# Optimization experiments

Measured on AMD Instinct MI355X. Metric: run time of the kernel, lower is better.

Reference implementation:

```python
import jax, jax.numpy as jnp
import numpy as np
from jax import lax

BOUNDARY_PER_ITERATION = [3, 2, 1, 0]  # boundary_width=4, boundary_iteration=4


def _cross_dilate(x):
    # grayscale dilation with 3x3 cross structuring element (max over center+4-neighbors)
    p = jnp.pad(x, ((0, 0), (0, 0), (1, 1), (1, 1)), constant_values=-jnp.inf)
    c = p[:, :, 1:-1, 1:-1]
    up = p[:, :, :-2, 1:-1]
    dn = p[:, :, 2:, 1:-1]
    lf = p[:, :, 1:-1, :-2]
    rt = p[:, :, 1:-1, 2:]
    return jnp.maximum(jnp.maximum(jnp.maximum(c, up), jnp.maximum(dn, lf)), rt)


def _full_erode(x):
    # grayscale erosion with full 3x3 structuring element (min over 3x3 window)
    return lax.reduce_window(x, jnp.inf, lax.min, (1, 1, 3, 3), (1, 1, 1, 1),
                             ((0, 0), (0, 0), (1, 1), (1, 1)))


def _box3_sum(x):
    # conv2d with all-ones 3x3 kernel, padding='same'
    return lax.reduce_window(x, 0.0, lax.add, (1, 1, 3, 3), (1, 1, 1, 1),
                             ((0, 0), (0, 0), (1, 1), (1, 1)))


def _find_boundaries(pred_f):
    return (_cross_dilate(pred_f) != _full_erode(pred_f)).astype(pred_f.dtype)


def _expand_boundaries(b, r):
    # dilation with diamond of radius r == r applications of cross dilation
    for _ in range(r):
        b = _cross_dilate(b)
    return b


def _gaussian_kernel_2d(n, std):
    i = np.arange(n, dtype=np.float64) - (n - 1) / 2.0
    g = np.exp(-(i ** 2) / (2.0 * std ** 2))
    g /= g.sum()
    return np.outer(g, g).astype(np.float32)  # cv2.getGaussianKernel outer product


def setup_inputs() -> dict:
    key = jax.random.key(0)
    k1, k2, k3 = jax.random.split(key, 3)
    n, c, h, w = 8, 19, 512, 512
    x = jax.random.normal(k1, (n, c, h, w), dtype=jnp.float32)
    means = jax.random.normal(k2, (c,), dtype=jnp.float32)
    std = jax.random.uniform(k3, (c,), dtype=jnp.float32) + 0.5  # positive variances
    gaussian_kernel = jnp.asarray(_gaussian_kernel_2d(7, 1.0))[None, None]  # (1,1,7,7)
    return {"x": x, "means": means, "std": std, "gaussian_kernel": gaussian_kernel}


def reference(x, means, std, gaussian_kernel):
    # max logits and prediction
    max_logits = jnp.max(x, axis=1, keepdims=True)           # (n,1,h,w)
    pred = jnp.argmax(x, axis=1, keepdims=True)              # (n,1,h,w) int
    sml = (max_logits - means[pred]) / std[pred]             # standardized max logits

    # boundary suppression
    pred_f = pred.astype(sml.dtype)
    boundaries = _find_boundaries(pred_f)
    for r in BOUNDARY_PER_ITERATION:
        expanded = _expand_boundaries(boundaries, r)
        nb_mask = (expanded == 0).astype(sml.dtype)
        sml_masked = sml * nb_mask
        sml_nb = _box3_sum(sml_masked)
        nb_cnt = _box3_sum(nb_mask)
        sml_avg = jnp.where(nb_cnt == 0, sml, sml_nb / jnp.where(nb_cnt == 0, 1.0, nb_cnt))
        sml = jnp.where(nb_mask == 0, sml_avg, sml)

    # dilated smoothing (gaussian conv, padding same)
    sml = lax.conv_general_dilated(sml, gaussian_kernel, (1, 1), 'SAME',
                                   dimension_numbers=('NCHW', 'OIHW', 'NCHW'))
    return sml, pred
```

## Files before the change

kernel.cpp:

```cpp
#include <hip/hip_runtime.h>
#include <cstdint>
#include <cstddef>

#define W_ 512
#define H_ 512
#define N_ 8
#define C_ 19
#define HW_ (W_*H_)
#define NPIX_ (N_*HW_)

#define TS  32
#define SR  46
#define SC  48
#define BR  52

typedef float   f32x4 __attribute__((ext_vector_type(4)));
typedef uint8_t u8x4  __attribute__((ext_vector_type(4)));
typedef unsigned long long u64;

__global__ __launch_bounds__(256) void k_argmax_sml(
    const float* __restrict__ x, const float* __restrict__ means,
    const float* __restrict__ stdv, float* __restrict__ sml,
    uint8_t* __restrict__ pred8, float* __restrict__ predf)
{
    __shared__ float xs[C_ * 1024];
    __shared__ float ms[C_], rs[C_];
    const int tid = threadIdx.x;
    if (tid < C_) {
        ms[tid] = means[tid];
        rs[tid] = __builtin_amdgcn_rcpf(stdv[tid]);
    }

    const int chunk = blockIdx.x;
    const int n   = chunk >> 8;
    const int p0  = (chunk & 255) << 10;
    const int wv  = tid >> 6, lane = tid & 63;
    const float* xg = x + (size_t)n * C_ * HW_ + p0;

    int cLo = wv * 5;
    int cHi = cLo + 5 > C_ ? C_ : cLo + 5;
    for (int c = cLo; c < cHi; ++c) {
        const float* g = xg + (size_t)c * HW_ + lane * 4;
        #pragma unroll
        for (int t = 0; t < 4; ++t) {
            __builtin_amdgcn_global_load_lds(
                (const __attribute__((address_space(1))) void*)(g + t * 256),
                (__attribute__((address_space(3))) void*)&xs[c * 1024 + t * 256],
                16, 0, 0);
        }
    }
    __syncthreads();

    const f32x4* xv = (const f32x4*)xs;
    f32x4 mv = xv[tid];
    int i0 = 0, i1 = 0, i2 = 0, i3 = 0;
    #pragma unroll
    for (int c = 1; c < C_; ++c) {
        f32x4 v = xv[c * 256 + tid];
        if (v[0] > mv[0]) { mv[0] = v[0]; i0 = c; }
        if (v[1] > mv[1]) { mv[1] = v[1]; i1 = c; }
        if (v[2] > mv[2]) { mv[2] = v[2]; i2 = c; }
        if (v[3] > mv[3]) { mv[3] = v[3]; i3 = c; }
    }
    const int pix = chunk * 1024 + tid * 4;
    f32x4 s, pf; u8x4 pc;
    s[0] = (mv[0] - ms[i0]) * rs[i0];  pf[0] = (float)i0;  pc[0] = (uint8_t)i0;
    s[1] = (mv[1] - ms[i1]) * rs[i1];  pf[1] = (float)i1;  pc[1] = (uint8_t)i1;
    s[2] = (mv[2] - ms[i2]) * rs[i2];  pf[2] = (float)i2;  pc[2] = (uint8_t)i2;
    s[3] = (mv[3] - ms[i3]) * rs[i3];  pf[3] = (float)i3;  pc[3] = (uint8_t)i3;
    *(f32x4*)(sml + pix) = s;
    *(u8x4*)(pred8 + pix) = pc;
    __builtin_nontemporal_store(pf, (f32x4*)(predf + pix));
}

__global__ __launch_bounds__(256) void k_bnd(
    const uint8_t* __restrict__ pred8, u64* __restrict__ bndM)
{
    int gid  = blockIdx.x * 256 + threadIdx.x;
    int lane = gid & 63;
    int wave = gid >> 6;
    int w = wave & 7;
    int y = (wave >> 3) & 511;
    int n = wave >> 12;
    int xx = w * 64 + lane;
    const uint8_t* pc = pred8 + (size_t)n * HW_ + y * W_ + xx;
    int c = pc[0];
    bool u = y > 0, d = y < H_-1, l = xx > 0, r = xx < W_-1;
    int up = u ? pc[-W_] : c;
    int dn = d ? pc[ W_] : c;
    int lf = l ? pc[-1]  : c;
    int rt = r ? pc[ 1]  : c;
    int mx = max(max(c, up), max(dn, max(lf, rt)));
    int mn = min(min(c, up), min(dn, min(lf, rt)));
    int c00 = (u && l) ? pc[-W_-1] : c;
    int c01 = (u && r) ? pc[-W_+1] : c;
    int c10 = (d && l) ? pc[ W_-1] : c;
    int c11 = (d && r) ? pc[ W_+1] : c;
    mn = min(mn, min(min(c00, c01), min(c10, c11)));
    u64 m = __ballot(mx != mn);
    if (lane == 0) bndM[((size_t)n * 512 + y) * 8 + w] = m;
}

__global__ __launch_bounds__(256) void k_fused(
    const float* __restrict__ sml_g, const u64* __restrict__ bndM,
    const float* __restrict__ gk, float* __restrict__ out)
{
    __shared__ float smlA[SR*SC];
    __shared__ float smlB[SR*SC];
    __shared__ u64 M0[BR], E1[BR], E2[BR], E3[BR], VM[BR];
    __shared__ u64 NBM[4][BR];
    __shared__ float g7[7];
    __shared__ int tACT;

    const int tid = threadIdx.x;
    const int bx = blockIdx.x, by = blockIdx.y, n = blockIdx.z;
    const int tx0 = bx * TS, ty0 = by * TS;
    const float* sg = sml_g + (size_t)n * HW_;

    if (tid == 0) tACT = 0;
    if (tid < 7) g7[tid] = gk[21 + tid] / sqrtf(gk[24]);

    if (tid < BR) {
        int gy = ty0 + tid - 10;
        int bx0 = tx0 - 10;
        u64 m = 0, vm = 0;
        if (gy >= 0 && gy < H_) {
            const u64* row = bndM + ((size_t)n * 512 + gy) * 8;
            int sft = bx0 & 63;
            int wi  = bx0 >> 6;
            u64 w0 = (wi >= 0) ? row[wi] : 0ULL;
            u64 w1 = (wi + 1 <= 7) ? row[wi + 1] : 0ULL;
            m = sft ? ((w0 >> sft) | (w1 << (64 - sft))) : w0;
            int lo = bx0 < 0 ? -bx0 : 0;
            int hi = (512 - bx0) < BR ? (512 - bx0) : BR;
            if (hi > lo) vm = ((1ULL << (hi - lo)) - 1ULL) << lo;
        }
        M0[tid] = m;
        VM[tid] = vm;
    }

    if (bx > 0 && bx < (W_/TS - 1)) {
        for (int s = tid; s < SR * (SC/4); s += 256) {
            int ly = s / (SC/4), j = s - ly * (SC/4);
            int gy = ty0 + ly - 7;
            f32x4 v = {0.f, 0.f, 0.f, 0.f};
            if ((unsigned)gy < (unsigned)H_)
                v = *(const f32x4*)(sg + (size_t)gy * W_ + (tx0 - 8) + j * 4);
            *(f32x4*)&smlA[ly * SC + j * 4] = v;
        }
    } else {
        for (int s = tid; s < SR * SC; s += 256) {
            int ly = s / SC, lx = s - ly * SC;
            int gy = ty0 + ly - 7, gx = tx0 + lx - 8;
            float v = 0.f;
            if ((unsigned)gy < (unsigned)H_ && (unsigned)gx < (unsigned)W_)
                v = sg[(size_t)gy * W_ + gx];
            smlA[ly * SC + lx] = v;
        }
    }
    __syncthreads();

    if (tid < BR) {
        u64 a = M0[tid], u = tid > 0 ? M0[tid-1] : 0, d = tid < BR-1 ? M0[tid+1] : 0;
        E1[tid] = a | (a << 1) | (a >> 1) | u | d;
    }
    __syncthreads();
    if (tid < BR) {
        u64 a = E1[tid], u = tid > 0 ? E1[tid-1] : 0, d = tid < BR-1 ? E1[tid+1] : 0;
        E2[tid] = a | (a << 1) | (a >> 1) | u | d;
    }
    __syncthreads();
    if (tid < BR) {
        u64 a = E2[tid], u = tid > 0 ? E2[tid-1] : 0, d = tid < BR-1 ? E2[tid+1] : 0;
        E3[tid] = a | (a << 1) | (a >> 1) | u | d;
    }
    __syncthreads();
    {
        int r = tid >> 6, i = tid & 63;
        if (i < BR) {
            u64 e = (r == 0) ? M0[i] : (r == 1) ? E1[i] : (r == 2) ? E2[i] : E3[i];
            NBM[r][i] = ~e & VM[i];
        }
    }
    __syncthreads();

    u64 actRow = 0;
    if (tid < SR) {
        int bi = tid + 3;
        u64 U = NBM[0][bi-1] | NBM[0][bi] | NBM[0][bi+1];
        u64 A = (U >> 1) | (U >> 2) | (U >> 3);
        int lo = tx0 == 0 ? 8 : 0;
        int hi = tx0 == (W_-TS) ? 40 : SC;
        u64 CV = (hi - lo >= 64) ? ~0ULL : (((1ULL << (hi - lo)) - 1ULL) << lo);
        actRow = A & CV;
        int gy = ty0 + tid - 7;
        if ((unsigned)gy >= (unsigned)H_) actRow = 0;
        if (actRow) tACT = 1;
    }
    __syncthreads();

    if (tACT) {
        #pragma unroll
        for (int k = 0; k < 4; ++k) {
            const int r = 3 - k;
            const u64 colmask = ((1ULL << (44 - 2*k)) - 1ULL) << (2 + k);
            u64 mwork = 0;
            if (tid >= 1 + k && tid < 45 - k && tid < SR)
                mwork = actRow & colmask;
            u64 mm = mwork;
            while (mm) {
                int lx = __ffsll(mm) - 1; mm &= mm - 1;
                int bi = tid + 3, sh = lx + 1;
                u64 fu = (NBM[r][bi-1] >> sh) & 7ULL;
                u64 fc = (NBM[r][bi  ] >> sh) & 7ULL;
                u64 fd = (NBM[r][bi+1] >> sh) & 7ULL;
                float c = smlA[tid*SC + lx];
                float o;
                if (((fc >> 1) & 1ULL) || !(fu | fc | fd)) {
                    o = c;
                } else {
                    int cnt = __popcll(fu) + __popcll(fc) + __popcll(fd);
                    float sum = 0.f;
                    const float* r0 = &smlA[(tid-1)*SC + lx];
                    const float* r1 = &smlA[(tid  )*SC + lx];
                    const float* r2 = &smlA[(tid+1)*SC + lx];
                    if (fu & 1) sum += r0[-1];
                    if (fu & 2) sum += r0[0];
                    if (fu & 4) sum += r0[1];
                    if (fc & 1) sum += r1[-1];
                    if (fc & 4) sum += r1[1];
                    if (fd & 1) sum += r2[-1];
                    if (fd & 2) sum += r2[0];
                    if (fd & 4) sum += r2[1];
                    o = sum / (float)cnt;
                }
                smlB[tid*SC + lx] = o;
            }
            __syncthreads();
            mm = mwork;
            while (mm) {
                int lx = __ffsll(mm) - 1; mm &= mm - 1;
                smlA[tid*SC + lx] = smlB[tid*SC + lx];
            }
            __syncthreads();
        }
    }

    float* htmp = smlB;
    for (int s = tid; s < 38 * 32; s += 256) {
        int hy = s >> 5, hx = s & 31;
        const float* p = &smlA[(hy + 4)*SC + (hx + 5)];
        htmp[hy*33 + hx] = g7[0]*p[0] + g7[1]*p[1] + g7[2]*p[2] + g7[3]*p[3]
                         + g7[4]*p[4] + g7[5]*p[5] + g7[6]*p[6];
    }
    __syncthreads();
    for (int s = tid; s < TS*TS; s += 256) {
        int oy = s >> 5, ox = s & 31;
        const float* p = &htmp[oy*33 + ox];
        float a = g7[0]*p[0]   + g7[1]*p[33]  + g7[2]*p[66]  + g7[3]*p[99]
                + g7[4]*p[132] + g7[5]*p[165] + g7[6]*p[198];
        out[(size_t)n*HW_ + (size_t)(ty0 + oy)*W_ + (tx0 + ox)] = a;
    }
}

extern "C" void kernel_launch(void* const* d_in, const int* in_sizes, int n_in,
                              void* d_out, int out_size, void* d_ws, size_t ws_size,
                              hipStream_t stream)
{
    const float* x     = (const float*)d_in[0];
    const float* means = (const float*)d_in[1];
    const float* stdv  = (const float*)d_in[2];
    const float* gk    = (const float*)d_in[3];
    float* out_sml  = (float*)d_out;
    float* out_pred = (float*)d_out + NPIX_;

    char* ws = (char*)d_ws;
    float*   sml   = (float*)(ws);
    uint8_t* pred8 = (uint8_t*)(ws + 8388608);
    u64*     bndM  = (u64*)(ws + 10485760);

    k_argmax_sml<<<NPIX_/1024, 256, 0, stream>>>(x, means, stdv, sml, pred8, out_pred);
    k_bnd<<<NPIX_/256, 256, 0, stream>>>(pred8, bndM);
    dim3 fgrd(W_/TS, H_/TS, N_);
    k_fused<<<fgrd, 256, 0, stream>>>(sml, bndM, gk, out_sml);
}
```

Before: 51.92 us.

## Add early-exit fast path for boundary-free tiles and halve argmax chunk size

```diff
diff --git a/kernel.cpp b/kernel.cpp
--- a/kernel.cpp
+++ b/kernel.cpp
@@ -15,7 +15,8 @@
 #define BR  52
 
 typedef float   f32x4 __attribute__((ext_vector_type(4)));
-typedef uint8_t u8x4  __attribute__((ext_vector_type(4)));
+typedef float   f32x2 __attribute__((ext_vector_type(2)));
+typedef uint8_t u8x2  __attribute__((ext_vector_type(2)));
 typedef unsigned long long u64;
 
 __global__ __launch_bounds__(256) void k_argmax_sml(
@@ -23,7 +24,7 @@
     const float* __restrict__ stdv, float* __restrict__ sml,
     uint8_t* __restrict__ pred8, float* __restrict__ predf)
 {
-    __shared__ float xs[C_ * 1024];
+    __shared__ float xs[C_ * 512];
     __shared__ float ms[C_], rs[C_];
     const int tid = threadIdx.x;
     if (tid < C_) {
@@ -32,8 +33,8 @@
     }
 
     const int chunk = blockIdx.x;
-    const int n   = chunk >> 8;
-    const int p0  = (chunk & 255) << 10;
+    const int n   = chunk >> 9;
+    const int p0  = (chunk & 511) << 9;
     const int wv  = tid >> 6, lane = tid & 63;
     const float* xg = x + (size_t)n * C_ * HW_ + p0;
 
@@ -42,35 +43,31 @@
     for (int c = cLo; c < cHi; ++c) {
         const float* g = xg + (size_t)c * HW_ + lane * 4;
         #pragma unroll
-        for (int t = 0; t < 4; ++t) {
+        for (int t = 0; t < 2; ++t) {
             __builtin_amdgcn_global_load_lds(
                 (const __attribute__((address_space(1))) void*)(g + t * 256),
-                (__attribute__((address_space(3))) void*)&xs[c * 1024 + t * 256],
+                (__attribute__((address_space(3))) void*)&xs[c * 512 + t * 256],
                 16, 0, 0);
         }
     }
     __syncthreads();
 
-    const f32x4* xv = (const f32x4*)xs;
-    f32x4 mv = xv[tid];
-    int i0 = 0, i1 = 0, i2 = 0, i3 = 0;
+    const f32x2* xv = (const f32x2*)xs;
+    f32x2 mv = xv[tid];
+    int i0 = 0, i1 = 0;
     #pragma unroll
     for (int c = 1; c < C_; ++c) {
-        f32x4 v = xv[c * 256 + tid];
+        f32x2 v = xv[c * 256 + tid];
         if (v[0] > mv[0]) { mv[0] = v[0]; i0 = c; }
         if (v[1] > mv[1]) { mv[1] = v[1]; i1 = c; }
-        if (v[2] > mv[2]) { mv[2] = v[2]; i2 = c; }
-        if (v[3] > mv[3]) { mv[3] = v[3]; i3 = c; }
-    }
-    const int pix = chunk * 1024 + tid * 4;
-    f32x4 s, pf; u8x4 pc;
+    }
+    const int pix = chunk * 512 + tid * 2;
+    f32x2 s, pf; u8x2 pc;
     s[0] = (mv[0] - ms[i0]) * rs[i0];  pf[0] = (float)i0;  pc[0] = (uint8_t)i0;
     s[1] = (mv[1] - ms[i1]) * rs[i1];  pf[1] = (float)i1;  pc[1] = (uint8_t)i1;
-    s[2] = (mv[2] - ms[i2]) * rs[i2];  pf[2] = (float)i2;  pc[2] = (uint8_t)i2;
-    s[3] = (mv[3] - ms[i3]) * rs[i3];  pf[3] = (float)i3;  pc[3] = (uint8_t)i3;
-    *(f32x4*)(sml + pix) = s;
-    *(u8x4*)(pred8 + pix) = pc;
-    __builtin_nontemporal_store(pf, (f32x4*)(predf + pix));
+    *(f32x2*)(sml + pix) = s;
+    *(u8x2*)(pred8 + pix) = pc;
+    __builtin_nontemporal_store(pf, (f32x2*)(predf + pix));
 }
 
 __global__ __launch_bounds__(256) void k_bnd(
@@ -138,6 +135,55 @@
         M0[tid] = m;
         VM[tid] = vm;
     }
+    __syncthreads();
+
+    u64 actRow = 0;
+    if (tid < SR) {
+        int bi = tid + 3;
+        u64 nbU = ~M0[bi-1] & VM[bi-1];
+        u64 nbC = ~M0[bi  ] & VM[bi  ];
+        u64 nbD = ~M0[bi+1] & VM[bi+1];
+        u64 U = nbU | nbC | nbD;
+        u64 A = (U >> 1) | (U >> 2) | (U >> 3);
+        int lo = tx0 == 0 ? 8 : 0;
+        int hi = tx0 == (W_-TS) ? 40 : SC;
+        u64 CV = (hi - lo >= 64) ? ~0ULL : (((1ULL << (hi - lo)) - 1ULL) << lo);
+        actRow = A & CV;
+        int gy = ty0 + tid - 7;
+        if ((unsigned)gy >= (unsigned)H_) actRow = 0;
+        if (actRow) tACT = 1;
+    }
+    __syncthreads();
+
+    if (!tACT) {
+        for (int s = tid; s < 38 * 10; s += 256) {
+            int q  = s / 10;
+            int ly = 4 + q, lx4 = s - q * 10;
+            int gy = ty0 + ly - 7;
+            int gx = tx0 - 4 + lx4 * 4;
+            f32x4 v = {0.f, 0.f, 0.f, 0.f};
+            if ((unsigned)gy < (unsigned)H_ && (unsigned)gx < (unsigned)W_)
+                v = *(const f32x4*)(sg + (size_t)gy * W_ + gx);
+            *(f32x4*)&smlA[ly * SC + 4 + lx4 * 4] = v;
+        }
+        __syncthreads();
+        float* htmp = smlB;
+        for (int s = tid; s < 38 * 32; s += 256) {
+            int hy = s >> 5, hx = s & 31;
+            const float* p = &smlA[(hy + 4)*SC + (hx + 5)];
+            htmp[hy*33 + hx] = g7[0]*p[0] + g7[1]*p[1] + g7[2]*p[2] + g7[3]*p[3]
+                             + g7[4]*p[4] + g7[5]*p[5] + g7[6]*p[6];
+        }
+        __syncthreads();
+        for (int s = tid; s < TS*TS; s += 256) {
+            int oy = s >> 5, ox = s & 31;
+            const float* p = &htmp[oy*33 + ox];
+            float a = g7[0]*p[0]   + g7[1]*p[33]  + g7[2]*p[66]  + g7[3]*p[99]
+                    + g7[4]*p[132] + g7[5]*p[165] + g7[6]*p[198];
+            out[(size_t)n*HW_ + (size_t)(ty0 + oy)*W_ + (tx0 + ox)] = a;
+        }
+        return;
+    }
 
     if (bx > 0 && bx < (W_/TS - 1)) {
         for (int s = tid; s < SR * (SC/4); s += 256) {
@@ -184,66 +230,49 @@
     }
     __syncthreads();
 
-    u64 actRow = 0;
-    if (tid < SR) {
-        int bi = tid + 3;
-        u64 U = NBM[0][bi-1] | NBM[0][bi] | NBM[0][bi+1];
-        u64 A = (U >> 1) | (U >> 2) | (U >> 3);
-        int lo = tx0 == 0 ? 8 : 0;
-        int hi = tx0 == (W_-TS) ? 40 : SC;
-        u64 CV = (hi - lo >= 64) ? ~0ULL : (((1ULL << (hi - lo)) - 1ULL) << lo);
-        actRow = A & CV;
-        int gy = ty0 + tid - 7;
-        if ((unsigned)gy >= (unsigned)H_) actRow = 0;
-        if (actRow) tACT = 1;
-    }
-    __syncthreads();
-
-    if (tACT) {
-        #pragma unroll
-        for (int k = 0; k < 4; ++k) {
-            const int r = 3 - k;
-            const u64 colmask = ((1ULL << (44 - 2*k)) - 1ULL) << (2 + k);
-            u64 mwork = 0;
-            if (tid >= 1 + k && tid < 45 - k && tid < SR)
-                mwork = actRow & colmask;
-            u64 mm = mwork;
-            while (mm) {
-                int lx = __ffsll(mm) - 1; mm &= mm - 1;
-                int bi = tid + 3, sh = lx + 1;
-                u64 fu = (NBM[r][bi-1] >> sh) & 7ULL;
-                u64 fc = (NBM[r][bi  ] >> sh) & 7ULL;
-                u64 fd = (NBM[r][bi+1] >> sh) & 7ULL;
-                float c = smlA[tid*SC + lx];
-                float o;
-                if (((fc >> 1) & 1ULL) || !(fu | fc | fd)) {
-                    o = c;
-                } else {
-                    int cnt = __popcll(fu) + __popcll(fc) + __popcll(fd);
-                    float sum = 0.f;
-                    const float* r0 = &smlA[(tid-1)*SC + lx];
-                    const float* r1 = &smlA[(tid  )*SC + lx];
-                    const float* r2 = &smlA[(tid+1)*SC + lx];
-                    if (fu & 1) sum += r0[-1];
-                    if (fu & 2) sum += r0[0];
-                    if (fu & 4) sum += r0[1];
-                    if (fc & 1) sum += r1[-1];
-                    if (fc & 4) sum += r1[1];
-                    if (fd & 1) sum += r2[-1];
-                    if (fd & 2) sum += r2[0];
-                    if (fd & 4) sum += r2[1];
-                    o = sum / (float)cnt;
-                }
-                smlB[tid*SC + lx] = o;
+    #pragma unroll
+    for (int k = 0; k < 4; ++k) {
+        const int r = 3 - k;
+        const u64 colmask = ((1ULL << (44 - 2*k)) - 1ULL) << (2 + k);
+        u64 mwork = 0;
+        if (tid >= 1 + k && tid < 45 - k && tid < SR)
+            mwork = actRow & colmask;
+        u64 mm = mwork;
+        while (mm) {
+            int lx = __ffsll(mm) - 1; mm &= mm - 1;
+            int bi = tid + 3, sh = lx + 1;
+            u64 fu = (NBM[r][bi-1] >> sh) & 7ULL;
+            u64 fc = (NBM[r][bi  ] >> sh) & 7ULL;
+            u64 fd = (NBM[r][bi+1] >> sh) & 7ULL;
+            float c = smlA[tid*SC + lx];
+            float o;
+            if (((fc >> 1) & 1ULL) || !(fu | fc | fd)) {
+                o = c;
+            } else {
+                int cnt = __popcll(fu) + __popcll(fc) + __popcll(fd);
+                float sum = 0.f;
+                const float* r0 = &smlA[(tid-1)*SC + lx];
+                const float* r1 = &smlA[(tid  )*SC + lx];
+                const float* r2 = &smlA[(tid+1)*SC + lx];
+                if (fu & 1) sum += r0[-1];
+                if (fu & 2) sum += r0[0];
+                if (fu & 4) sum += r0[1];
+                if (fc & 1) sum += r1[-1];
+                if (fc & 4) sum += r1[1];
+                if (fd & 1) sum += r2[-1];
+                if (fd & 2) sum += r2[0];
+                if (fd & 4) sum += r2[1];
+                o = sum / (float)cnt;
             }
-            __syncthreads();
-            mm = mwork;
-            while (mm) {
-                int lx = __ffsll(mm) - 1; mm &= mm - 1;
-                smlA[tid*SC + lx] = smlB[tid*SC + lx];
-            }
-            __syncthreads();
-        }
+            smlB[tid*SC + lx] = o;
+        }
+        __syncthreads();
+        mm = mwork;
+        while (mm) {
+            int lx = __ffsll(mm) - 1; mm &= mm - 1;
+            smlA[tid*SC + lx] = smlB[tid*SC + lx];
+        }
+        __syncthreads();
     }
 
     float* htmp = smlB;
@@ -279,7 +308,7 @@
     uint8_t* pred8 = (uint8_t*)(ws + 8388608);
     u64*     bndM  = (u64*)(ws + 10485760);
 
-    k_argmax_sml<<<NPIX_/1024, 256, 0, stream>>>(x, means, stdv, sml, pred8, out_pred);
+    k_argmax_sml<<<NPIX_/512, 256, 0, stream>>>(x, means, stdv, sml, pred8, out_pred);
     k_bnd<<<NPIX_/256, 256, 0, stream>>>(pred8, bndM);
     dim3 fgrd(W_/TS, H_/TS, N_);
     k_fused<<<fgrd, 256, 0, stream>>>(sml, bndM, gk, out_sml);
```

After: 51.34 us. Within noise of the previous version (-1.1%).
